# Performance work log

Hardware: AMD Instinct MI355X
Metric: run time of the kernel (lower is better)

Reference implementation:

```python
import jax, jax.numpy as jnp
import numpy as np

AXIAL_WEIGHT = 1.0
N_NODES = 1_000_000
N_ELEM = 2_000_000


def setup_inputs() -> dict:
    key = jax.random.key(0)
    ks = jax.random.split(key, 12)
    N, E = N_NODES, N_ELEM
    pred_raw = jax.random.normal(ks[0], (N, 3), jnp.float32)
    u_c = jax.random.uniform(ks[1], (1,), jnp.float32) + 0.5
    theta_c = jax.random.uniform(ks[2], (1,), jnp.float32) + 0.5
    connectivity = jax.random.randint(ks[3], (E, 2), 0, N, jnp.int32)
    # lengths / section properties bounded away from zero (1/L^3 appears)
    elem_lengths = jax.random.uniform(ks[4], (E,), jnp.float32) + 0.5
    prop_E = jax.random.uniform(ks[5], (E,), jnp.float32) + 1.0
    prop_A = jax.random.uniform(ks[6], (E,), jnp.float32) + 0.5
    prop_I22 = jax.random.uniform(ks[7], (E,), jnp.float32) + 0.5
    ang = jax.random.uniform(ks[8], (E,), jnp.float32) * (2.0 * np.pi)
    # columns: [cos, 0, sin] -- forward reads cols 0 and 2
    elem_directions = jnp.stack([jnp.cos(ang), jnp.zeros_like(ang), jnp.sin(ang)], axis=1)
    F_ext = jax.random.normal(ks[9], (N, 3), jnp.float32)
    bc_disp = (jax.random.uniform(ks[10], (N, 1)) < 0.05).astype(jnp.float32)
    bc_rot = (jax.random.uniform(ks[11], (N, 1)) < 0.05).astype(jnp.float32)
    return {
        "pred_raw": pred_raw, "u_c": u_c, "theta_c": theta_c,
        "elem_lengths": elem_lengths, "prop_E": prop_E, "prop_A": prop_A,
        "prop_I22": prop_I22, "elem_directions": elem_directions,
        "F_ext": F_ext, "bc_disp": bc_disp, "bc_rot": bc_rot,
        "connectivity": connectivity,
    }


def reference(pred_raw, u_c, theta_c, elem_lengths, prop_E, prop_A, prop_I22,
              elem_directions, F_ext, bc_disp, bc_rot, connectivity):
    n_nodes = pred_raw.shape[0]
    # physical displacements: [ux*u_c, uz*u_c, th*theta_c]
    scale = jnp.concatenate([u_c, u_c, theta_c])  # [3]
    u_phys = pred_raw * scale[None, :]

    nA = connectivity[:, 0]
    nB = connectivity[:, 1]
    c = elem_directions[:, 0]
    s = elem_directions[:, 2]
    L = elem_lengths
    EA = prop_E * prop_A
    EI = prop_E * prop_I22

    uA = u_phys[nA]  # [E,3] gather
    uB = u_phys[nB]
    u_A = c * uA[:, 0] + s * uA[:, 1]
    w_A = -s * uA[:, 0] + c * uA[:, 1]
    th_A = -uA[:, 2]
    u_B = c * uB[:, 0] + s * uB[:, 1]
    w_B = -s * uB[:, 0] + c * uB[:, 1]
    th_B = -uB[:, 2]

    ea_l = EA / L * AXIAL_WEIGHT
    ei_l = EI / L
    ei_l2 = EI / L**2
    ei_l3 = EI / L**3

    # analytic K_loc @ d_local (K_loc is the standard 6x6 beam stiffness)
    dw = w_A - w_B
    f0 = ea_l * (u_A - u_B)
    f1 = 12.0 * ei_l3 * dw + 6.0 * ei_l2 * (th_A + th_B)
    f2 = 6.0 * ei_l2 * dw + 4.0 * ei_l * th_A + 2.0 * ei_l * th_B
    f3 = -f0
    f4 = -f1
    f5 = 6.0 * ei_l2 * dw + 2.0 * ei_l * th_A + 4.0 * ei_l * th_B

    fA = jnp.stack([c * f0 - s * f1, s * f0 + c * f1, -f2], axis=1)  # [E,3]
    fB = jnp.stack([c * f3 - s * f4, s * f3 + c * f4, -f5], axis=1)

    F_int = jax.ops.segment_sum(
        jnp.concatenate([fA, fB], axis=0),
        jnp.concatenate([nA, nB], axis=0),
        num_segments=n_nodes)  # [N,3] scatter-add

    R = F_int - F_ext
    free_mask = jnp.concatenate([1.0 - bc_disp, 1.0 - bc_disp, 1.0 - bc_rot], axis=1)
    R_free = R * free_mask
    F_free = F_ext * free_mask
    F_norm_sq = jnp.maximum(jnp.sum(F_free**2), 1e-30)
    loss = jnp.sum(R_free**2) / F_norm_sq  # single graph -> n_graphs = 1
    return loss
```

## Files before the change

### kernel.cpp

```cpp
#include <hip/hip_runtime.h>
#include <hip/hip_fp16.h>


#define SPANC  4096
#define NBC    256
#define CURP   16
#define FTH    1024
#define FBE    2048
#define ATH    1024
#define CB     96
#define QSCALE 8192.0f
#define QINV   1.220703125e-4f

struct F3 { float x, y, z; };

__device__ __forceinline__ uint2 packrec(float fx, float fy, float fz, int local) {
    unsigned short hx = __half_as_ushort(__float2half(fx));
    unsigned short hy = __half_as_ushort(__float2half(fy));
    unsigned short hz = __half_as_ushort(__float2half(fz));
    return make_uint2(((unsigned)hy << 16) | hx, ((unsigned)local << 16) | hz);
}

__device__ __forceinline__ int block_incl_scan(int v, int* wsum, int lane, int wv) {
    #pragma unroll
    for (int off = 1; off < 64; off <<= 1) {
        int t = __shfl_up(v, off, 64);
        if (lane >= off) v += t;
    }
    if (lane == 63) wsum[wv] = v;
    __syncthreads();
    if (wv == 0) {
        int w = (lane < 16) ? wsum[lane] : 0;
        #pragma unroll
        for (int off = 1; off < 16; off <<= 1) {
            int t = __shfl_up(w, off, 64);
            if (lane >= off) w += t;
        }
        if (lane < 16) wsum[lane] = w;
    }
    __syncthreads();
    return v + ((wv > 0) ? wsum[wv - 1] : 0);
}

__global__ void __launch_bounds__(1024)
upack_kernel(const float* __restrict__ pred, const float* __restrict__ u_c,
             const float* __restrict__ theta_c, uint2* __restrict__ up, int N) {
    int i = blockIdx.x * 1024 + threadIdx.x;
    if (i >= N) return;
    float uc = u_c[0], tc = theta_c[0];
    float x = __builtin_nontemporal_load(&pred[3 * i + 0]) * uc;
    float y = __builtin_nontemporal_load(&pred[3 * i + 1]) * uc;
    float z = __builtin_nontemporal_load(&pred[3 * i + 2]) * tc;
    unsigned hx = __half_as_ushort(__float2half(x));
    unsigned hy = __half_as_ushort(__float2half(y));
    unsigned hz = __half_as_ushort(__float2half(z));
    up[i] = make_uint2((hy << 16) | hx, hz);
}

__global__ void __launch_bounds__(1024)
count_kernel(const long long* __restrict__ conn, int* __restrict__ rows,
             int cs, int ce) {
    __shared__ int h[NBC];
    int tid = threadIdx.x;
    if (tid < NBC) h[tid] = 0;
    __syncthreads();
    int stride = gridDim.x * 1024;
    for (int e = cs + blockIdx.x * 1024 + tid; e < ce; e += stride) {
        long long v = __builtin_nontemporal_load(conn + e);
        int na = (int)(unsigned)((unsigned long long)v & 0xFFFFFFFFull);
        int nb = (int)(unsigned)((unsigned long long)v >> 32);
        atomicAdd(&h[na >> 12], 1);
        atomicAdd(&h[nb >> 12], 1);
    }
    __syncthreads();
    if (tid < NBC)
        __builtin_nontemporal_store(h[tid], &rows[blockIdx.x * NBC + tid]);
}

__global__ void __launch_bounds__(1024)
scan_kernel(const int* __restrict__ rows, int* __restrict__ cursor,
            int* __restrict__ base, double* __restrict__ accSlots,
            int isFirst) {
    __shared__ int wsum[16];
    int tid = threadIdx.x, lane = tid & 63, wv = tid >> 6;
    int c = 0;
    if (tid < NBC) {
        #pragma unroll 4
        for (int r = 0; r < CB; ++r) c += rows[r * NBC + tid];
    }
    int incl = block_incl_scan(c, wsum, lane, wv);
    if (tid < NBC) {
        base[tid + 1] = incl;
        cursor[tid * CURP] = incl - c;
    }
    if (tid == 0) base[0] = 0;
    if (isFirst && tid < 512) accSlots[tid] = 0.0;
}

__global__ void __launch_bounds__(1024)
fill_kernel(const long long* __restrict__ conn,
            const uint2* __restrict__ upk,
            const float* __restrict__ len,
            const float* __restrict__ pE,
            const float* __restrict__ pA,
            const float* __restrict__ pI,
            const float* __restrict__ dir,
            uint2* __restrict__ arena,
            int* __restrict__ cursor,
            int cs, int ce) {
    __shared__ uint2         slab[2 * FBE];
    __shared__ unsigned char sbk [2 * FBE];
    __shared__ int hist [NBC];
    __shared__ int boff [NBC];
    __shared__ int astart[NBC];
    __shared__ int wsum [16];

    int tid = threadIdx.x, lane = tid & 63, wv = tid >> 6;

    if (tid < NBC) hist[tid] = 0;
    __syncthreads();

    int bs = cs + blockIdx.x * FBE;
    int be = bs + FBE; if (be > ce) be = ce;

    unsigned sv[4];
    uint2    rc[4];

    #pragma unroll
    for (int j = 0; j < 2; ++j) {
        int e = bs + j * FTH + tid;
        unsigned sa = 0xFFFFFFFFu, sb = 0xFFFFFFFFu;
        if (e < be) {
            long long cv = __builtin_nontemporal_load(conn + e);
            int na = (int)(unsigned)((unsigned long long)cv & 0xFFFFFFFFull);
            int nb = (int)(unsigned)((unsigned long long)cv >> 32);

            uint2 ua = upk[na];
            uint2 ub = upk[nb];

            float c  = __builtin_nontemporal_load(&dir[3 * e + 0]);
            float s  = __builtin_nontemporal_load(&dir[3 * e + 2]);
            float L  = __builtin_nontemporal_load(&len[e]);
            float Ee = __builtin_nontemporal_load(&pE[e]);
            float EA = Ee * __builtin_nontemporal_load(&pA[e]);
            float EI = Ee * __builtin_nontemporal_load(&pI[e]);

            float a0 = __half2float(__ushort_as_half((unsigned short)(ua.x & 0xFFFFu)));
            float a1 = __half2float(__ushort_as_half((unsigned short)(ua.x >> 16)));
            float a2 = __half2float(__ushort_as_half((unsigned short)(ua.y & 0xFFFFu)));
            float b0 = __half2float(__ushort_as_half((unsigned short)(ub.x & 0xFFFFu)));
            float b1 = __half2float(__ushort_as_half((unsigned short)(ub.x >> 16)));
            float b2 = __half2float(__ushort_as_half((unsigned short)(ub.y & 0xFFFFu)));

            float u_A  =  c * a0 + s * a1;
            float w_A  = -s * a0 + c * a1;
            float th_A = -a2;
            float u_B  =  c * b0 + s * b1;
            float w_B  = -s * b0 + c * b1;
            float th_B = -b2;

            float invL  = 1.0f / L;
            float ea_l  = EA * invL;
            float ei_l  = EI * invL;
            float ei_l2 = ei_l  * invL;
            float ei_l3 = ei_l2 * invL;

            float dw = w_A - w_B;
            float f0 = ea_l * (u_A - u_B);
            float f1 = 12.0f * ei_l3 * dw + 6.0f * ei_l2 * (th_A + th_B);
            float f2 = 6.0f * ei_l2 * dw + 4.0f * ei_l * th_A + 2.0f * ei_l * th_B;
            float f5 = 6.0f * ei_l2 * dw + 2.0f * ei_l * th_A + 4.0f * ei_l * th_B;

            float fA0 = c * f0 - s * f1;
            float fA1 = s * f0 + c * f1;

            int bkA = na >> 12;
            int rA  = atomicAdd(&hist[bkA], 1);
            sa = ((unsigned)rA << 8) | (unsigned)bkA;
            rc[2 * j + 0] = packrec(fA0, fA1, -f2, na & 4095);

            int bkB = nb >> 12;
            int rB  = atomicAdd(&hist[bkB], 1);
            sb = ((unsigned)rB << 8) | (unsigned)bkB;
            rc[2 * j + 1] = packrec(-fA0, -fA1, -f5, nb & 4095);
        }
        sv[2 * j + 0] = sa;
        sv[2 * j + 1] = sb;
    }
    __syncthreads();

    int h = (tid < NBC) ? hist[tid] : 0;
    if (tid < NBC && h) astart[tid] = atomicAdd(&cursor[tid * CURP], h);
    int iT = block_incl_scan(h, wsum, lane, wv);
    if (tid < NBC) boff[tid] = iT - h;
    __syncthreads();

    #pragma unroll
    for (int r = 0; r < 4; ++r) {
        unsigned s2 = sv[r];
        if (s2 != 0xFFFFFFFFu) {
            int bk = (int)(s2 & 255u);
            int rk = (int)(s2 >> 8);
            int slot = boff[bk] + rk;
            slab[slot] = rc[r];
            sbk[slot]  = (unsigned char)bk;
        }
    }
    __syncthreads();

    int tot = boff[NBC - 1] + hist[NBC - 1];
    for (int i = tid; i < tot; i += FTH) {
        int bk = sbk[i];
        uint2 r2 = slab[i];
        unsigned long long v = ((unsigned long long)r2.y << 32) | (unsigned long long)r2.x;
        __builtin_nontemporal_store(v,
            (unsigned long long*)&arena[astart[bk] + (i - boff[bk])]);
    }
}

__global__ void __launch_bounds__(1024)
accum_kernel(const unsigned long long* __restrict__ arena,
             const int* __restrict__ base,
             const float* __restrict__ Fext,
             const float* __restrict__ bcd,
             const float* __restrict__ bcr,
             double* __restrict__ accSlots,
             int* __restrict__ fintI,
             unsigned short* __restrict__ fint16,
             int N, int isFirst, int isLast, int mode) {
    __shared__ int tile[SPANC * 3];
    __shared__ double sn[16], sd[16];

    int tid = threadIdx.x, lane = tid & 63, wv = tid >> 6;
    int b = blockIdx.x;
    int nodeLo = b * SPANC;
    int gBase = nodeLo * 3;
    int gMax  = 3 * N;

    if (isFirst) {
        for (int i = tid; i < SPANC * 3; i += ATH) tile[i] = 0;
    } else if (mode == 1) {
        for (int i = tid; i < SPANC * 3; i += ATH) {
            int g = gBase + i;
            tile[i] = (g < gMax) ? __builtin_nontemporal_load(&fintI[g]) : 0;
        }
    } else {
        for (int i = tid; i < SPANC * 3; i += ATH) {
            int g = gBase + i;
            tile[i] = (g < gMax)
                ? __float2int_rn(__half2float(__ushort_as_half(
                      __builtin_nontemporal_load(&fint16[g]))) * QSCALE)
                : 0;
        }
    }
    __syncthreads();

    int s0 = base[b];
    int s1 = base[b + 1];
    for (int i = s0 + tid; i < s1; i += ATH) {
        unsigned long long rv = __builtin_nontemporal_load(arena + i);
        unsigned lo = (unsigned)(rv & 0xFFFFFFFFull);
        unsigned hi = (unsigned)(rv >> 32);
        float fx = __half2float(__ushort_as_half((unsigned short)(lo & 0xFFFFu)));
        float fy = __half2float(__ushort_as_half((unsigned short)(lo >> 16)));
        float fz = __half2float(__ushort_as_half((unsigned short)(hi & 0xFFFFu)));
        int local = (int)(hi >> 16);
        atomicAdd(&tile[local * 3 + 0], __float2int_rn(fx * QSCALE));
        atomicAdd(&tile[local * 3 + 1], __float2int_rn(fy * QSCALE));
        atomicAdd(&tile[local * 3 + 2], __float2int_rn(fz * QSCALE));
    }
    __syncthreads();

    if (!isLast) {
        if (mode == 1) {
            for (int i = tid; i < SPANC * 3; i += ATH) {
                int g = gBase + i;
                if (g < gMax) __builtin_nontemporal_store(tile[i], &fintI[g]);
            }
        } else {
            for (int i = tid; i < SPANC * 3; i += ATH) {
                int g = gBase + i;
                if (g < gMax)
                    __builtin_nontemporal_store(
                        __half_as_ushort(__float2half((float)tile[i] * QINV)),
                        &fint16[g]);
            }
        }
        return;
    }

    int spanCnt = N - nodeLo;
    if (spanCnt > SPANC) spanCnt = SPANC;

    double num = 0.0, den = 0.0;
    for (int l = tid; l < spanCnt; l += ATH) {
        int n = nodeLo + l;
        float md = 1.0f - __builtin_nontemporal_load(&bcd[n]);
        float mr = 1.0f - __builtin_nontemporal_load(&bcr[n]);
        float e0 = __builtin_nontemporal_load(&Fext[3 * n + 0]);
        float e1 = __builtin_nontemporal_load(&Fext[3 * n + 1]);
        float e2 = __builtin_nontemporal_load(&Fext[3 * n + 2]);
        float t0 = (float)tile[l * 3 + 0] * QINV;
        float t1 = (float)tile[l * 3 + 1] * QINV;
        float t2 = (float)tile[l * 3 + 2] * QINV;
        float r0 = (t0 - e0) * md;
        float r1 = (t1 - e1) * md;
        float r2 = (t2 - e2) * mr;
        float g0 = e0 * md;
        float g1 = e1 * md;
        float g2 = e2 * mr;
        num += (double)r0 * r0 + (double)r1 * r1 + (double)r2 * r2;
        den += (double)g0 * g0 + (double)g1 * g1 + (double)g2 * g2;
    }
    #pragma unroll
    for (int off = 32; off > 0; off >>= 1) {
        num += __shfl_down(num, off, 64);
        den += __shfl_down(den, off, 64);
    }
    if (lane == 0) { sn[wv] = num; sd[wv] = den; }
    __syncthreads();
    if (tid == 0) {
        double tn = 0.0, td = 0.0;
        #pragma unroll
        for (int w = 0; w < 16; ++w) { tn += sn[w]; td += sd[w]; }
        double* slot = accSlots + (size_t)(b & 63) * 8;
        atomicAdd(&slot[0], tn);
        atomicAdd(&slot[1], td);
    }
}

__global__ void final_kernel(const double* __restrict__ accSlots,
                             float* __restrict__ out) {
    int t = threadIdx.x;
    double n = accSlots[t * 8 + 0];
    double d = accSlots[t * 8 + 1];
    #pragma unroll
    for (int off = 32; off > 0; off >>= 1) {
        n += __shfl_down(n, off, 64);
        d += __shfl_down(d, off, 64);
    }
    if (t == 0) {
        if (d < 1e-30) d = 1e-30;
        out[0] = (float)(n / d);
    }
}

static inline size_t align256(size_t x) { return (x + 255) & ~(size_t)255; }

extern "C" void kernel_launch(void* const* d_in, const int* in_sizes, int n_in,
                              void* d_out, int out_size, void* d_ws, size_t ws_size,
                              hipStream_t stream) {
    const float* pred    = (const float*)d_in[0];
    const float* u_c     = (const float*)d_in[1];
    const float* theta_c = (const float*)d_in[2];
    const float* len     = (const float*)d_in[3];
    const float* pE      = (const float*)d_in[4];
    const float* pA      = (const float*)d_in[5];
    const float* pI      = (const float*)d_in[6];
    const float* dir     = (const float*)d_in[7];
    const float* Fext    = (const float*)d_in[8];
    const float* bcd     = (const float*)d_in[9];
    const float* bcr     = (const float*)d_in[10];
    const long long* conn = (const long long*)d_in[11];

    int N = in_sizes[0] / 3;
    int E = in_sizes[3];
    int NBc = (N + SPANC - 1) / SPANC;

    size_t oCur   = 4096;
    size_t oBase  = oCur + (size_t)NBC * CURP * 4;
    size_t oU     = align256(oBase + 4 * (NBC + 1));
    size_t upB    = (size_t)N * 8;
    size_t oFint0 = align256(oU + upB);
    size_t rowsBytes = (size_t)CB * NBC * 4;

    const int cfgK[6] = {1, 2, 3, 4, 6, 8};
    const int cfgM[6] = {0, 2, 2, 2, 2, 2};
    int K = 8, mode = 2;
    size_t oF = oFint0, oA = oFint0;
    for (int t = 0; t < 6; ++t) {
        int Kc = cfgK[t], Mc = cfgM[t];
        size_t chunkE = (size_t)(E + Kc - 1) / Kc;
        size_t fsz = (Kc > 1) ? (size_t)3 * N * (Mc == 1 ? 4 : 2) : 0;
        size_t oAt = align256(oFint0 + fsz);
        size_t arenaB = 2 * chunkE * 8;
        if (arenaB < rowsBytes) arenaB = rowsBytes;
        size_t need = oAt + arenaB;
        if (need <= ws_size || t == 5) {
            K = Kc; mode = Mc; oF = oFint0; oA = oAt;
            if (need <= ws_size) break;
        }
    }

    int chunkElems = (E + K - 1) / K;

    double*             accSlots = (double*)d_ws;
    int*                cursor   = (int*)((char*)d_ws + oCur);
    int*                base     = (int*)((char*)d_ws + oBase);
    uint2*              upk      = (uint2*)((char*)d_ws + oU);
    int*                fintI    = (int*)((char*)d_ws + oF);
    unsigned short*     fint16   = (unsigned short*)((char*)d_ws + oF);
    uint2*              arena    = (uint2*)((char*)d_ws + oA);
    unsigned long long* arenaLL  = (unsigned long long*)arena;
    int*                rows     = (int*)arena;

    upack_kernel<<<(N + 1023) / 1024, 1024, 0, stream>>>(pred, u_c, theta_c, upk, N);

    for (int c = 0; c < K; ++c) {
        int cs = c * chunkElems;
        if (cs >= E) break;
        int ce = cs + chunkElems;
        if (ce > E) ce = E;
        int NT = (ce - cs + FBE - 1) / FBE;

        int isFirst = (c == 0);
        int isLast  = (ce == E);

        count_kernel<<<CB, 1024, 0, stream>>>(conn, rows, cs, ce);
        scan_kernel<<<1, 1024, 0, stream>>>(rows, cursor, base, accSlots, isFirst);
        fill_kernel<<<NT, FTH, 0, stream>>>(
            conn, upk, len, pE, pA, pI, dir, arena, cursor, cs, ce);
        accum_kernel<<<NBc, ATH, 0, stream>>>(
            arenaLL, base, Fext, bcd, bcr, accSlots,
            fintI, fint16, N, isFirst, isLast, mode);
    }

    final_kernel<<<1, 64, 0, stream>>>(accSlots, (float*)d_out);
}
```

Before: 223.5 us.

## Fuse count/unpack, scan all chunks once, overlap fill with previous accum

The unpack and per-chunk count kernels merge into one launch that histograms all four fixed chunks at once. A single scan kernel now computes cursors and bases for every chunk. The per-chunk fill and accumulate steps are combined into a mid kernel whose blocks either fill chunk c or accumulate chunk c-1 into double-buffered arenas. This cuts launch count and serialization between stages, but it fixes the chunk count at four, always goes through the fp16 intermediate F_int, and needs more workspace for the second arena.

Measured after the change: 260.3 us. +16.5%, slower.

```diff
diff --git a/kernel.cpp b/kernel.cpp
--- a/kernel.cpp
+++ b/kernel.cpp
@@ -4,15 +4,25 @@
 
 #define SPANC  4096
 #define NBC    256
-#define CURP   16
+#define CURP   4
 #define FTH    1024
 #define FBE    2048
-#define ATH    1024
 #define CB     96
+#define NCHUNK 4
+#define BASEI  272
 #define QSCALE 8192.0f
 #define QINV   1.220703125e-4f
 
-struct F3 { float x, y, z; };
+#define SMEM_BYTES 49408
+#define FO_SLAB 0
+#define FO_SBK  32768
+#define FO_HIST 36864
+#define FO_BOFF 37888
+#define FO_AST  38912
+#define FO_WSUM 39936
+#define AO_TILE 0
+#define AO_SN   49152
+#define AO_SD   49280
 
 __device__ __forceinline__ uint2 packrec(float fx, float fy, float fz, int local) {
     unsigned short hx = __half_as_ushort(__float2half(fx));
@@ -43,84 +53,94 @@
 }
 
 __global__ void __launch_bounds__(1024)
-upack_kernel(const float* __restrict__ pred, const float* __restrict__ u_c,
-             const float* __restrict__ theta_c, uint2* __restrict__ up, int N) {
-    int i = blockIdx.x * 1024 + threadIdx.x;
-    if (i >= N) return;
-    float uc = u_c[0], tc = theta_c[0];
-    float x = __builtin_nontemporal_load(&pred[3 * i + 0]) * uc;
-    float y = __builtin_nontemporal_load(&pred[3 * i + 1]) * uc;
-    float z = __builtin_nontemporal_load(&pred[3 * i + 2]) * tc;
-    unsigned hx = __half_as_ushort(__float2half(x));
-    unsigned hy = __half_as_ushort(__float2half(y));
-    unsigned hz = __half_as_ushort(__float2half(z));
-    up[i] = make_uint2((hy << 16) | hx, hz);
-}
-
-__global__ void __launch_bounds__(1024)
-count_kernel(const long long* __restrict__ conn, int* __restrict__ rows,
-             int cs, int ce) {
-    __shared__ int h[NBC];
+upcnt_kernel(const float* __restrict__ pred, const float* __restrict__ u_c,
+             const float* __restrict__ theta_c, uint2* __restrict__ up,
+             int N, int upG,
+             const long long* __restrict__ conn, int* __restrict__ rows,
+             int E, int CE) {
+    __shared__ int h[NCHUNK][NBC];
     int tid = threadIdx.x;
-    if (tid < NBC) h[tid] = 0;
-    __syncthreads();
-    int stride = gridDim.x * 1024;
-    for (int e = cs + blockIdx.x * 1024 + tid; e < ce; e += stride) {
+    int bid = blockIdx.x;
+
+    if (bid < upG) {
+        int i = bid * 1024 + tid;
+        if (i < N) {
+            float uc = u_c[0], tc = theta_c[0];
+            float x = __builtin_nontemporal_load(&pred[3 * i + 0]) * uc;
+            float y = __builtin_nontemporal_load(&pred[3 * i + 1]) * uc;
+            float z = __builtin_nontemporal_load(&pred[3 * i + 2]) * tc;
+            unsigned hx = __half_as_ushort(__float2half(x));
+            unsigned hy = __half_as_ushort(__float2half(y));
+            unsigned hz = __half_as_ushort(__float2half(z));
+            up[i] = make_uint2((hy << 16) | hx, hz);
+        }
+        return;
+    }
+
+    int blk = bid - upG;
+    h[tid >> 8][tid & 255] = 0;
+    __syncthreads();
+    int stride = CB * 1024;
+    int ce2 = 2 * CE, ce3 = 3 * CE;
+    for (int e = blk * 1024 + tid; e < E; e += stride) {
         long long v = __builtin_nontemporal_load(conn + e);
         int na = (int)(unsigned)((unsigned long long)v & 0xFFFFFFFFull);
         int nb = (int)(unsigned)((unsigned long long)v >> 32);
-        atomicAdd(&h[na >> 12], 1);
-        atomicAdd(&h[nb >> 12], 1);
-    }
-    __syncthreads();
-    if (tid < NBC)
-        __builtin_nontemporal_store(h[tid], &rows[blockIdx.x * NBC + tid]);
+        int c = (e >= ce2) ? ((e >= ce3) ? 3 : 2) : ((e >= CE) ? 1 : 0);
+        atomicAdd(&h[c][na >> 12], 1);
+        atomicAdd(&h[c][nb >> 12], 1);
+    }
+    __syncthreads();
+    int c = tid >> 8, b = tid & 255;
+    __builtin_nontemporal_store(h[c][b], &rows[(c * CB + blk) * NBC + b]);
 }
 
 __global__ void __launch_bounds__(1024)
-scan_kernel(const int* __restrict__ rows, int* __restrict__ cursor,
-            int* __restrict__ base, double* __restrict__ accSlots,
-            int isFirst) {
+scan4_kernel(const int* __restrict__ rows, int* __restrict__ cursors,
+             int* __restrict__ bases, double* __restrict__ accSlots) {
     __shared__ int wsum[16];
+    __shared__ int segend[NCHUNK];
     int tid = threadIdx.x, lane = tid & 63, wv = tid >> 6;
-    int c = 0;
-    if (tid < NBC) {
-        #pragma unroll 4
-        for (int r = 0; r < CB; ++r) c += rows[r * NBC + tid];
-    }
-    int incl = block_incl_scan(c, wsum, lane, wv);
-    if (tid < NBC) {
-        base[tid + 1] = incl;
-        cursor[tid * CURP] = incl - c;
-    }
-    if (tid == 0) base[0] = 0;
-    if (isFirst && tid < 512) accSlots[tid] = 0.0;
-}
-
-__global__ void __launch_bounds__(1024)
-fill_kernel(const long long* __restrict__ conn,
-            const uint2* __restrict__ upk,
-            const float* __restrict__ len,
-            const float* __restrict__ pE,
-            const float* __restrict__ pA,
-            const float* __restrict__ pI,
-            const float* __restrict__ dir,
-            uint2* __restrict__ arena,
-            int* __restrict__ cursor,
-            int cs, int ce) {
-    __shared__ uint2         slab[2 * FBE];
-    __shared__ unsigned char sbk [2 * FBE];
-    __shared__ int hist [NBC];
-    __shared__ int boff [NBC];
-    __shared__ int astart[NBC];
-    __shared__ int wsum [16];
+    int c = tid >> 8, b = tid & 255;
+    int v = 0;
+    #pragma unroll 4
+    for (int r = 0; r < CB; ++r) v += rows[(c * CB + r) * NBC + b];
+    int incl = block_incl_scan(v, wsum, lane, wv);
+    if (b == 255) segend[c] = incl;
+    __syncthreads();
+    int segoff = (c > 0) ? segend[c - 1] : 0;
+    int inclSeg = incl - segoff;
+    int* base_c = bases + c * BASEI;
+    base_c[b + 1] = inclSeg;
+    if (b == 0) base_c[0] = 0;
+    cursors[(c * NBC + b) * CURP] = inclSeg - v;
+    if (tid < 512) accSlots[tid] = 0.0;
+}
+
+__device__ __forceinline__ void fill_body(
+    char* smem,
+    const long long* __restrict__ conn,
+    const uint2* __restrict__ upk,
+    const float* __restrict__ len,
+    const float* __restrict__ pE,
+    const float* __restrict__ pA,
+    const float* __restrict__ pI,
+    const float* __restrict__ dir,
+    uint2* __restrict__ arena,
+    int* __restrict__ cursor,
+    int cs, int ce, int bid) {
+    uint2*         slab   = (uint2*)(smem + FO_SLAB);
+    unsigned char* sbk    = (unsigned char*)(smem + FO_SBK);
+    int*           hist   = (int*)(smem + FO_HIST);
+    int*           boff   = (int*)(smem + FO_BOFF);
+    int*           astart = (int*)(smem + FO_AST);
+    int*           wsum   = (int*)(smem + FO_WSUM);
 
     int tid = threadIdx.x, lane = tid & 63, wv = tid >> 6;
-
     if (tid < NBC) hist[tid] = 0;
     __syncthreads();
 
-    int bs = cs + blockIdx.x * FBE;
+    int bs = cs + bid * FBE;
     int be = bs + FBE; if (be > ce) be = ce;
 
     unsigned sv[4];
@@ -218,34 +238,29 @@
     }
 }
 
-__global__ void __launch_bounds__(1024)
-accum_kernel(const unsigned long long* __restrict__ arena,
-             const int* __restrict__ base,
-             const float* __restrict__ Fext,
-             const float* __restrict__ bcd,
-             const float* __restrict__ bcr,
-             double* __restrict__ accSlots,
-             int* __restrict__ fintI,
-             unsigned short* __restrict__ fint16,
-             int N, int isFirst, int isLast, int mode) {
-    __shared__ int tile[SPANC * 3];
-    __shared__ double sn[16], sd[16];
+__device__ __forceinline__ void accum_body(
+    char* smem,
+    const unsigned long long* __restrict__ arena,
+    const int* __restrict__ base,
+    const float* __restrict__ Fext,
+    const float* __restrict__ bcd,
+    const float* __restrict__ bcr,
+    double* __restrict__ accSlots,
+    unsigned short* __restrict__ fint16,
+    int N, int isFirst, int isLast, int b) {
+    int*    tile = (int*)(smem + AO_TILE);
+    double* sn   = (double*)(smem + AO_SN);
+    double* sd   = (double*)(smem + AO_SD);
 
     int tid = threadIdx.x, lane = tid & 63, wv = tid >> 6;
-    int b = blockIdx.x;
     int nodeLo = b * SPANC;
     int gBase = nodeLo * 3;
     int gMax  = 3 * N;
 
     if (isFirst) {
-        for (int i = tid; i < SPANC * 3; i += ATH) tile[i] = 0;
-    } else if (mode == 1) {
-        for (int i = tid; i < SPANC * 3; i += ATH) {
-            int g = gBase + i;
-            tile[i] = (g < gMax) ? __builtin_nontemporal_load(&fintI[g]) : 0;
-        }
+        for (int i = tid; i < SPANC * 3; i += FTH) tile[i] = 0;
     } else {
-        for (int i = tid; i < SPANC * 3; i += ATH) {
+        for (int i = tid; i < SPANC * 3; i += FTH) {
             int g = gBase + i;
             tile[i] = (g < gMax)
                 ? __float2int_rn(__half2float(__ushort_as_half(
@@ -257,7 +272,7 @@
 
     int s0 = base[b];
     int s1 = base[b + 1];
-    for (int i = s0 + tid; i < s1; i += ATH) {
+    for (int i = s0 + tid; i < s1; i += FTH) {
         unsigned long long rv = __builtin_nontemporal_load(arena + i);
         unsigned lo = (unsigned)(rv & 0xFFFFFFFFull);
         unsigned hi = (unsigned)(rv >> 32);
@@ -272,19 +287,12 @@
     __syncthreads();
 
     if (!isLast) {
-        if (mode == 1) {
-            for (int i = tid; i < SPANC * 3; i += ATH) {
-                int g = gBase + i;
-                if (g < gMax) __builtin_nontemporal_store(tile[i], &fintI[g]);
-            }
-        } else {
-            for (int i = tid; i < SPANC * 3; i += ATH) {
-                int g = gBase + i;
-                if (g < gMax)
-                    __builtin_nontemporal_store(
-                        __half_as_ushort(__float2half((float)tile[i] * QINV)),
-                        &fint16[g]);
-            }
+        for (int i = tid; i < SPANC * 3; i += FTH) {
+            int g = gBase + i;
+            if (g < gMax)
+                __builtin_nontemporal_store(
+                    __half_as_ushort(__float2half((float)tile[i] * QINV)),
+                    &fint16[g]);
         }
         return;
     }
@@ -293,7 +301,7 @@
     if (spanCnt > SPANC) spanCnt = SPANC;
 
     double num = 0.0, den = 0.0;
-    for (int l = tid; l < spanCnt; l += ATH) {
+    for (int l = tid; l < spanCnt; l += FTH) {
         int n = nodeLo + l;
         float md = 1.0f - __builtin_nontemporal_load(&bcd[n]);
         float mr = 1.0f - __builtin_nontemporal_load(&bcr[n]);
@@ -329,6 +337,49 @@
     }
 }
 
+__global__ void __launch_bounds__(1024)
+fill_kernel(const long long* __restrict__ conn, const uint2* __restrict__ upk,
+            const float* __restrict__ len, const float* __restrict__ pE,
+            const float* __restrict__ pA, const float* __restrict__ pI,
+            const float* __restrict__ dir, uint2* __restrict__ arena,
+            int* __restrict__ cursor, int cs, int ce) {
+    __shared__ __align__(16) char smem[SMEM_BYTES];
+    fill_body(smem, conn, upk, len, pE, pA, pI, dir, arena, cursor, cs, ce,
+              blockIdx.x);
+}
+
+__global__ void __launch_bounds__(1024)
+accum_kernel(const unsigned long long* __restrict__ arena,
+             const int* __restrict__ base, const float* __restrict__ Fext,
+             const float* __restrict__ bcd, const float* __restrict__ bcr,
+             double* __restrict__ accSlots, unsigned short* __restrict__ fint16,
+             int N, int isFirst, int isLast) {
+    __shared__ __align__(16) char smem[SMEM_BYTES];
+    accum_body(smem, arena, base, Fext, bcd, bcr, accSlots, fint16, N,
+               isFirst, isLast, blockIdx.x);
+}
+
+__global__ void __launch_bounds__(1024)
+mid_kernel(const long long* __restrict__ conn, const uint2* __restrict__ upk,
+           const float* __restrict__ len, const float* __restrict__ pE,
+           const float* __restrict__ pA, const float* __restrict__ pI,
+           const float* __restrict__ dir,
+           uint2* __restrict__ arenaF, int* __restrict__ cursorF,
+           int csF, int ceF, int NTF,
+           const unsigned long long* __restrict__ arenaA,
+           const int* __restrict__ baseA,
+           const float* __restrict__ Fext, const float* __restrict__ bcd,
+           const float* __restrict__ bcr, double* __restrict__ accSlots,
+           unsigned short* __restrict__ fint16, int N, int isFirstA) {
+    __shared__ __align__(16) char smem[SMEM_BYTES];
+    if ((int)blockIdx.x < NTF)
+        fill_body(smem, conn, upk, len, pE, pA, pI, dir, arenaF, cursorF,
+                  csF, ceF, blockIdx.x);
+    else
+        accum_body(smem, arenaA, baseA, Fext, bcd, bcr, accSlots, fint16, N,
+                   isFirstA, 0, blockIdx.x - NTF);
+}
+
 __global__ void final_kernel(const double* __restrict__ accSlots,
                              float* __restrict__ out) {
     int t = threadIdx.x;
@@ -366,63 +417,75 @@
     int N = in_sizes[0] / 3;
     int E = in_sizes[3];
     int NBc = (N + SPANC - 1) / SPANC;
-
-    size_t oCur   = 4096;
-    size_t oBase  = oCur + (size_t)NBC * CURP * 4;
-    size_t oU     = align256(oBase + 4 * (NBC + 1));
-    size_t upB    = (size_t)N * 8;
-    size_t oFint0 = align256(oU + upB);
-    size_t rowsBytes = (size_t)CB * NBC * 4;
-
-    const int cfgK[6] = {1, 2, 3, 4, 6, 8};
-    const int cfgM[6] = {0, 2, 2, 2, 2, 2};
-    int K = 8, mode = 2;
-    size_t oF = oFint0, oA = oFint0;
-    for (int t = 0; t < 6; ++t) {
-        int Kc = cfgK[t], Mc = cfgM[t];
-        size_t chunkE = (size_t)(E + Kc - 1) / Kc;
-        size_t fsz = (Kc > 1) ? (size_t)3 * N * (Mc == 1 ? 4 : 2) : 0;
-        size_t oAt = align256(oFint0 + fsz);
-        size_t arenaB = 2 * chunkE * 8;
-        if (arenaB < rowsBytes) arenaB = rowsBytes;
-        size_t need = oAt + arenaB;
-        if (need <= ws_size || t == 5) {
-            K = Kc; mode = Mc; oF = oFint0; oA = oAt;
-            if (need <= ws_size) break;
-        }
-    }
-
-    int chunkElems = (E + K - 1) / K;
+    int CE  = (E + NCHUNK - 1) / NCHUNK;
+    int nCh = (E + CE - 1) / CE;
+    int upG = (N + 1023) / 1024;
+
+    size_t oCur  = 4096;
+    size_t oBase = oCur + (size_t)NCHUNK * NBC * CURP * 4;
+    size_t oU    = align256(oBase + (size_t)NCHUNK * BASEI * 4);
+    size_t oFint = align256(oU + (size_t)N * 8);
+    size_t oA0   = align256(oFint + (size_t)3 * N * 2);
+    size_t arenaB = (size_t)2 * CE * 8;
+    size_t rowsB  = (size_t)NCHUNK * CB * NBC * 4;
+    size_t a0B    = (arenaB > rowsB) ? arenaB : rowsB;
+    size_t oA1    = align256(oA0 + a0B);
+    int fused = (oA1 + arenaB) <= ws_size;
 
     double*             accSlots = (double*)d_ws;
-    int*                cursor   = (int*)((char*)d_ws + oCur);
-    int*                base     = (int*)((char*)d_ws + oBase);
+    int*                cursors  = (int*)((char*)d_ws + oCur);
+    int*                bases    = (int*)((char*)d_ws + oBase);
     uint2*              upk      = (uint2*)((char*)d_ws + oU);
-    int*                fintI    = (int*)((char*)d_ws + oF);
-    unsigned short*     fint16   = (unsigned short*)((char*)d_ws + oF);
-    uint2*              arena    = (uint2*)((char*)d_ws + oA);
-    unsigned long long* arenaLL  = (unsigned long long*)arena;
-    int*                rows     = (int*)arena;
-
-    upack_kernel<<<(N + 1023) / 1024, 1024, 0, stream>>>(pred, u_c, theta_c, upk, N);
-
-    for (int c = 0; c < K; ++c) {
-        int cs = c * chunkElems;
-        if (cs >= E) break;
-        int ce = cs + chunkElems;
-        if (ce > E) ce = E;
-        int NT = (ce - cs + FBE - 1) / FBE;
-
-        int isFirst = (c == 0);
-        int isLast  = (ce == E);
-
-        count_kernel<<<CB, 1024, 0, stream>>>(conn, rows, cs, ce);
-        scan_kernel<<<1, 1024, 0, stream>>>(rows, cursor, base, accSlots, isFirst);
-        fill_kernel<<<NT, FTH, 0, stream>>>(
-            conn, upk, len, pE, pA, pI, dir, arena, cursor, cs, ce);
-        accum_kernel<<<NBc, ATH, 0, stream>>>(
-            arenaLL, base, Fext, bcd, bcr, accSlots,
-            fintI, fint16, N, isFirst, isLast, mode);
+    unsigned short*     fint16   = (unsigned short*)((char*)d_ws + oFint);
+    uint2*              arena0   = (uint2*)((char*)d_ws + oA0);
+    uint2*              arena1   = (uint2*)((char*)d_ws + oA1);
+    int*                rows     = (int*)arena0;
+
+    upcnt_kernel<<<upG + CB, 1024, 0, stream>>>(
+        pred, u_c, theta_c, upk, N, upG, conn, rows, E, CE);
+    scan4_kernel<<<1, 1024, 0, stream>>>(rows, cursors, bases, accSlots);
+
+    if (fused) {
+        {
+            int cs = 0, ce = (CE < E) ? CE : E;
+            int NT = (ce - cs + FBE - 1) / FBE;
+            fill_kernel<<<NT, FTH, 0, stream>>>(
+                conn, upk, len, pE, pA, pI, dir,
+                arena0, cursors + 0, 0, ce);
+        }
+        for (int c = 1; c < nCh; ++c) {
+            int cs = c * CE;
+            int ce = cs + CE; if (ce > E) ce = E;
+            int NT = (ce - cs + FBE - 1) / FBE;
+            uint2* aF = (c & 1) ? arena1 : arena0;
+            const unsigned long long* aA = (const unsigned long long*)
+                (((c - 1) & 1) ? arena1 : arena0);
+            mid_kernel<<<NT + NBc, FTH, 0, stream>>>(
+                conn, upk, len, pE, pA, pI, dir,
+                aF, cursors + (size_t)c * NBC * CURP, cs, ce, NT,
+                aA, bases + (size_t)(c - 1) * BASEI,
+                Fext, bcd, bcr, accSlots, fint16, N, (c - 1) == 0);
+        }
+        {
+            int last = nCh - 1;
+            const unsigned long long* aA = (const unsigned long long*)
+                ((last & 1) ? arena1 : arena0);
+            accum_kernel<<<NBc, FTH, 0, stream>>>(
+                aA, bases + (size_t)last * BASEI,
+                Fext, bcd, bcr, accSlots, fint16, N, last == 0, 1);
+        }
+    } else {
+        for (int c = 0; c < nCh; ++c) {
+            int cs = c * CE;
+            int ce = cs + CE; if (ce > E) ce = E;
+            int NT = (ce - cs + FBE - 1) / FBE;
+            fill_kernel<<<NT, FTH, 0, stream>>>(
+                conn, upk, len, pE, pA, pI, dir,
+                arena0, cursors + (size_t)c * NBC * CURP, cs, ce);
+            accum_kernel<<<NBc, FTH, 0, stream>>>(
+                (const unsigned long long*)arena0, bases + (size_t)c * BASEI,
+                Fext, bcd, bcr, accSlots, fint16, N, c == 0, c == nCh - 1);
+        }
     }
 
     final_kernel<<<1, 64, 0, stream>>>(accSlots, (float*)d_out);
```
